# Kernel optimization log

Hardware: AMD Instinct MI355X
Metric: run time of the kernel (lower is better)

## Reference

```python
import jax, jax.numpy as jnp
import numpy as np

HID = 64


def _lstm_cell(x, h, c, Wih, Whh, bih, bhh):
    # gates: [B, 4*HID], PyTorch LSTMCell gate order: i, f, g, o
    gates = x @ Wih.T + bih + h @ Whh.T + bhh
    i, f, g, o = jnp.split(gates, 4, axis=-1)
    c_new = jax.nn.sigmoid(f) * c + jax.nn.sigmoid(i) * jnp.tanh(g)
    h_new = jax.nn.sigmoid(o) * jnp.tanh(c_new)
    return h_new, c_new


def setup_inputs() -> dict:
    key = jax.random.key(0)
    ks = jax.random.split(key, 11)
    B = 131072
    s_in2 = 1.0 / np.sqrt(2.0)
    s_h = 1.0 / np.sqrt(HID)
    return {
        "train_agent": jax.random.normal(ks[0], (B, 20, 2), jnp.float32),
        "enc_Wih": jax.random.uniform(ks[1], (4 * HID, 2), jnp.float32, -s_h, s_h),
        "enc_Whh": jax.random.uniform(ks[2], (4 * HID, HID), jnp.float32, -s_h, s_h),
        "enc_bih": jax.random.uniform(ks[3], (4 * HID,), jnp.float32, -s_h, s_h),
        "enc_bhh": jax.random.uniform(ks[4], (4 * HID,), jnp.float32, -s_h, s_h),
        "dec_Wih": jax.random.uniform(ks[5], (4 * HID, HID), jnp.float32, -s_h, s_h),
        "dec_Whh": jax.random.uniform(ks[6], (4 * HID, HID), jnp.float32, -s_h, s_h),
        "dec_bih": jax.random.uniform(ks[7], (4 * HID,), jnp.float32, -s_h, s_h),
        "dec_bhh": jax.random.uniform(ks[8], (4 * HID,), jnp.float32, -s_h, s_h),
        "lin_W": jax.random.uniform(ks[9], (2, HID), jnp.float32, -s_h, s_h),
        "lin_b": jax.random.uniform(ks[10], (2,), jnp.float32, -s_h, s_h),
    }


def reference(train_agent, enc_Wih, enc_Whh, enc_bih, enc_bhh,
              dec_Wih, dec_Whh, dec_bih, dec_bhh, lin_W, lin_b):
    B = train_agent.shape[0]
    h0 = jnp.zeros((B, HID), train_agent.dtype)
    c0 = jnp.zeros((B, HID), train_agent.dtype)

    # Encoder: 20 sequential LSTMCell steps over [B, 20, 2]
    def enc_step(carry, x_t):
        h, c = carry
        h, c = _lstm_cell(x_t, h, c, enc_Wih, enc_Whh, enc_bih, enc_bhh)
        return (h, c), None

    xs = jnp.swapaxes(train_agent, 0, 1)  # [20, B, 2]
    (h, c), _ = jax.lax.scan(enc_step, (h0, c0), xs)

    # Decoder: 30 steps, feeding h back in as input; emit Linear(h)
    def dec_step(carry, _):
        h, c = carry
        h, c = _lstm_cell(h, h, c, dec_Wih, dec_Whh, dec_bih, dec_bhh)
        out = h @ lin_W.T + lin_b  # [B, 2]
        return (h, c), out

    (_, _), outs = jax.lax.scan(dec_step, (h, c), None, length=30)
    return jnp.swapaxes(outs, 0, 1)  # [B, 30, 2]
```

## Files before the change

kernel.cpp:

```cpp
#include <hip/hip_runtime.h>


#define LOG2E 1.44269504088896340736f
#define TWO_LOG2E 2.88539008177792681472f

typedef __attribute__((ext_vector_type(4))) short short4v;
typedef __attribute__((ext_vector_type(4))) float float4v;
typedef __attribute__((ext_vector_type(4))) unsigned int uint4v;
typedef _Float16 __attribute__((ext_vector_type(8))) half8v;

#if defined(__HIP_DEVICE_COMPILE__)
#define MFMAH(a, b, c) __builtin_amdgcn_mfma_f32_16x16x32_f16((a), (b), (c), 0, 0, 0)
#else
#define MFMAH(a, b, c) (c)
#endif

__device__ __forceinline__ float4v exp2v4(float4v x) {
  float4v r;
  r[0] = __builtin_amdgcn_exp2f(x[0]);
  r[1] = __builtin_amdgcn_exp2f(x[1]);
  r[2] = __builtin_amdgcn_exp2f(x[2]);
  r[3] = __builtin_amdgcn_exp2f(x[3]);
  return r;
}
__device__ __forceinline__ float4v rcpv4(float4v x) {
  float4v r;
  r[0] = __builtin_amdgcn_rcpf(x[0]);
  r[1] = __builtin_amdgcn_rcpf(x[1]);
  r[2] = __builtin_amdgcn_rcpf(x[2]);
  r[3] = __builtin_amdgcn_rcpf(x[3]);
  return r;
}

__device__ __forceinline__ void cellact(const float4v* a, float4v& c,
                                        short4v& hh) {
  const float4v one = {1.f, 1.f, 1.f, 1.f};
  const float4v clo = {-36.f, -36.f, -36.f, -36.f};
  const float4v chi = {36.f, 36.f, 36.f, 36.f};
  float4v Ei = exp2v4(a[0]);
  float4v Ef = exp2v4(a[1]);
  float4v Eg = exp2v4(a[2]);
  float4v Eo = exp2v4(a[3]);
  float4v t1 = one + Ei;
  float4v t2 = one + Eg;
  float4v t3 = one + Ef;
  float4v t4s = Eg * TWO_LOG2E - TWO_LOG2E;
  float4v P = t1 * t2;
  float4v num = c * P + t4s * t3;
  float4v cs = num * rcpv4(P * t3);
  c = cs;
  float4v cl = __builtin_elementwise_min(__builtin_elementwise_max(cs, clo), chi);
  float4v Ec = exp2v4(cl);
  float4v h = (Ec - one) * rcpv4((one + Ec) * (one + Eo));
#pragma unroll
  for (int r = 0; r < 4; ++r) {
    _Float16 hf = (_Float16)h[r];
    hh[r] = (short)__builtin_bit_cast(unsigned short, hf);
  }
}

__global__ __launch_bounds__(256, 3) void lstm_fused(
    const float* __restrict__ x,
    const float* __restrict__ eWih,
    const float* __restrict__ eWhh,
    const float* __restrict__ ebih,
    const float* __restrict__ ebhh,
    const float* __restrict__ dWih,
    const float* __restrict__ dWhh,
    const float* __restrict__ dbih,
    const float* __restrict__ dbhh,
    const float* __restrict__ linW,
    const float* __restrict__ linb,
    float* __restrict__ out,
    int B) {
  const int tid = threadIdx.x;
  const int w   = tid >> 6;
  const int l   = tid & 63;
  const int m   = l & 15;
  const int tg  = l >> 4;
  const int msk = m & 14;
  const int wslot = (((w << 2) | tg) ^ msk) << 2;
  const int bg  = blockIdx.x * 32;

  __shared__ __align__(16) unsigned short WL[10][256][8];
  __shared__ __align__(16) unsigned short Hh[2][32][64];
  __shared__ unsigned int Xs16[32][21];

  const half8v hz8 = {0, 0, 0, 0, 0, 0, 0, 0};
  const float4v zf = {0.f, 0.f, 0.f, 0.f};

  {
    const size_t xoff = (size_t)blockIdx.x * 1280;
    for (int i = tid; i < 640; i += 256) {
      int mm = i / 20, st = i - mm * 20;
      size_t g = xoff + (size_t)mm * 40 + st * 2;
      float xa = 0.f, xb = 0.f;
      if (g + 1 < (size_t)B * 40) { xa = x[g]; xb = x[g + 1]; }
      unsigned ua = __builtin_bit_cast(unsigned short, (_Float16)xa);
      unsigned ub = __builtin_bit_cast(unsigned short, (_Float16)xb);
      Xs16[mm][st] = (ub << 16) | ua;
    }
  }

  half8v eA2[4];
#pragma unroll
  for (int gi = 0; gi < 4; ++gi) {
    const float gsc = (gi == 2) ? TWO_LOG2E : -LOG2E;
    const int nA = m + 16 * (4 * gi + w);
#pragma unroll
    for (int q = 0; q < 2; ++q) {
      const float* wp = &eWhh[nA * 64 + 32 * q + 8 * tg];
      float4v w0 = *(const float4v*)wp;
      float4v w1 = *(const float4v*)(wp + 4);
      half8v hi;
#pragma unroll
      for (int e = 0; e < 4; ++e) {
        hi[e]     = (_Float16)(w0[e] * gsc);
        hi[4 + e] = (_Float16)(w1[e] * gsc);
      }
      *(half8v*)&WL[gi * 2 + q][tid][0] = hi;
    }
    half8v a2 = hz8;
    if (tg == 0) {
      a2[0] = (_Float16)(eWih[nA * 2 + 0] * gsc);
      a2[1] = (_Float16)(eWih[nA * 2 + 1] * gsc);
      a2[2] = (_Float16)((ebih[nA] + ebhh[nA]) * gsc);
    }
    eA2[gi] = a2;
  }

  __syncthreads();

  float4v c0 = {0.f, 0.f, 0.f, 0.f}, c1 = {0.f, 0.f, 0.f, 0.f};
  half8v b0[2] = {hz8, hz8}, b1[2] = {hz8, hz8};
  int p = 0;

#pragma unroll 1
  for (int st = 0; st < 20; ++st) {
    short4v hh0, hh1;
    {
      uint4v t; t[0] = Xs16[m][st]; t[1] = 0x3C00u; t[2] = 0u; t[3] = 0u;
      half8v bq2 = (tg == 0) ? __builtin_bit_cast(half8v, t) : hz8;
      float4v a0[4];
#pragma unroll
      for (int gi = 0; gi < 4; ++gi) {
        half8v f0 = *(const half8v*)&WL[gi * 2 + 0][tid][0];
        half8v f1 = *(const half8v*)&WL[gi * 2 + 1][tid][0];
        float4v a = MFMAH(eA2[gi], bq2, zf);
        a = MFMAH(f0, b0[0], a);
        a0[gi] = MFMAH(f1, b0[1], a);
      }
      cellact(a0, c0, hh0);
    }
    {
      uint4v t; t[0] = Xs16[m + 16][st]; t[1] = 0x3C00u; t[2] = 0u; t[3] = 0u;
      half8v bq2 = (tg == 0) ? __builtin_bit_cast(half8v, t) : hz8;
      float4v a1[4];
#pragma unroll
      for (int gi = 0; gi < 4; ++gi) {
        half8v f0 = *(const half8v*)&WL[gi * 2 + 0][tid][0];
        half8v f1 = *(const half8v*)&WL[gi * 2 + 1][tid][0];
        float4v a = MFMAH(eA2[gi], bq2, zf);
        a = MFMAH(f0, b1[0], a);
        a1[gi] = MFMAH(f1, b1[1], a);
      }
      cellact(a1, c1, hh1);
    }
    *(short4v*)&Hh[p][m][wslot]      = hh0;
    *(short4v*)&Hh[p][m + 16][wslot] = hh1;
    __syncthreads();
#pragma unroll
    for (int q = 0; q < 2; ++q) {
      const int rs = (((8 * q) | (2 * tg)) ^ msk) << 2;
      b0[q] = *(const half8v*)&Hh[p][m][rs];
      b1[q] = *(const half8v*)&Hh[p][m + 16][rs];
    }
    p ^= 1;
  }

  float4v dbsv[4];
#pragma unroll
  for (int gi = 0; gi < 4; ++gi) {
    const float gsc = (gi == 2) ? TWO_LOG2E : -LOG2E;
    const int nA = m + 16 * (4 * gi + w);
#pragma unroll
    for (int q = 0; q < 2; ++q) {
      const float* wpa = &dWih[nA * 64 + 32 * q + 8 * tg];
      const float* wpb = &dWhh[nA * 64 + 32 * q + 8 * tg];
      float4v a0v = *(const float4v*)wpa;
      float4v a1v = *(const float4v*)(wpa + 4);
      float4v b0v = *(const float4v*)wpb;
      float4v b1v = *(const float4v*)(wpb + 4);
      half8v hi;
#pragma unroll
      for (int e = 0; e < 4; ++e) {
        hi[e]     = (_Float16)((a0v[e] + b0v[e]) * gsc);
        hi[4 + e] = (_Float16)((a1v[e] + b1v[e]) * gsc);
      }
      *(half8v*)&WL[gi * 2 + q][tid][0] = hi;
    }
#pragma unroll
    for (int r = 0; r < 4; ++r) {
      const int n = 64 * gi + 16 * w + 4 * tg + r;
      dbsv[gi][r] = (dbih[n] + dbhh[n]) * gsc;
    }
  }
#pragma unroll
  for (int q = 0; q < 2; ++q) {
    half8v hi = hz8;
    if (m < 2) {
      const int k0 = 32 * q + 8 * tg;
#pragma unroll
      for (int e = 0; e < 4; ++e) {
        hi[e]     = (_Float16)linW[m * 64 + k0 + e];
        hi[4 + e] = (_Float16)linW[m * 64 + k0 + e + 4];
      }
    }
    *(half8v*)&WL[8 + q][tid][0] = hi;
  }
  float4v lbinit = {0.f, 0.f, 0.f, 0.f};
  if (tg == 0) { lbinit[0] = linb[0]; lbinit[1] = linb[1]; }
  __syncthreads();

#pragma unroll 1
  for (int st = 0; st < 30; ++st) {
    short4v hh0, hh1;
    {
      float4v a0[4];
#pragma unroll
      for (int gi = 0; gi < 4; ++gi) {
        half8v f0 = *(const half8v*)&WL[gi * 2 + 0][tid][0];
        half8v f1 = *(const half8v*)&WL[gi * 2 + 1][tid][0];
        float4v a = MFMAH(f0, b0[0], dbsv[gi]);
        a0[gi] = MFMAH(f1, b0[1], a);
      }
      cellact(a0, c0, hh0);
    }
    {
      float4v a1[4];
#pragma unroll
      for (int gi = 0; gi < 4; ++gi) {
        half8v f0 = *(const half8v*)&WL[gi * 2 + 0][tid][0];
        half8v f1 = *(const half8v*)&WL[gi * 2 + 1][tid][0];
        float4v a = MFMAH(f0, b1[0], dbsv[gi]);
        a1[gi] = MFMAH(f1, b1[1], a);
      }
      cellact(a1, c1, hh1);
    }
    *(short4v*)&Hh[p][m][wslot]      = hh0;
    *(short4v*)&Hh[p][m + 16][wslot] = hh1;
    __syncthreads();
#pragma unroll
    for (int q = 0; q < 2; ++q) {
      const int rs = (((8 * q) | (2 * tg)) ^ msk) << 2;
      b0[q] = *(const half8v*)&Hh[p][m][rs];
      b1[q] = *(const half8v*)&Hh[p][m + 16][rs];
    }
    if (w == 0) {
      half8v L0 = *(const half8v*)&WL[8][tid][0];
      half8v L1 = *(const half8v*)&WL[9][tid][0];
      float4v la = lbinit;
      la = MFMAH(L0, b0[0], la);
      la = MFMAH(L1, b0[1], la);
      if (l < 16 && (bg + l) < B) {
        size_t oidx = ((size_t)(bg + l) * 30 + st) * 2;
        *(float2*)&out[oidx] = make_float2(la[0], la[1]);
      }
    } else if (w == 1) {
      half8v L0 = *(const half8v*)&WL[8][tid][0];
      half8v L1 = *(const half8v*)&WL[9][tid][0];
      float4v la = lbinit;
      la = MFMAH(L0, b1[0], la);
      la = MFMAH(L1, b1[1], la);
      if (l < 16 && (bg + 16 + l) < B) {
        size_t oidx = ((size_t)(bg + 16 + l) * 30 + st) * 2;
        *(float2*)&out[oidx] = make_float2(la[0], la[1]);
      }
    }
    p ^= 1;
  }
}

extern "C" void kernel_launch(void* const* d_in, const int* in_sizes, int n_in,
                              void* d_out, int out_size, void* d_ws, size_t ws_size,
                              hipStream_t stream) {
  (void)n_in; (void)out_size; (void)d_ws; (void)ws_size;
  const float* x    = (const float*)d_in[0];
  const float* eWih = (const float*)d_in[1];
  const float* eWhh = (const float*)d_in[2];
  const float* ebih = (const float*)d_in[3];
  const float* ebhh = (const float*)d_in[4];
  const float* dWih = (const float*)d_in[5];
  const float* dWhh = (const float*)d_in[6];
  const float* dbih = (const float*)d_in[7];
  const float* dbhh = (const float*)d_in[8];
  const float* linW = (const float*)d_in[9];
  const float* linb = (const float*)d_in[10];

  const int B = in_sizes[0] / 40;
  const int grid = (B + 31) / 32;
  lstm_fused<<<grid, 256, 0, stream>>>(x, eWih, eWhh, ebih, ebhh,
                                       dWih, dWhh, dbih, dbhh, linW, linb,
                                       (float*)d_out, B);
}
```

Measured before the change: 432.6 us.

## Halve per-block batch to 16 rows and raise occupancy to four blocks

Each 256-thread block now handles 16 batch rows instead of 32, so each wave runs one MFMA/cell chain per step instead of two. This lowers register pressure, and the launch bound is raised from 3 to 4 blocks per SM. Decoder biases move from registers to a shared-memory array, and the linear-layer weights move to a compact LDS table. The trade-off is twice as many blocks, each redoing the weight conversion into LDS, and less independent work per wave to hide MFMA and transcendental latency between barriers.

```diff
diff --git a/kernel.cpp b/kernel.cpp
--- a/kernel.cpp
+++ b/kernel.cpp
@@ -59,7 +59,7 @@
   }
 }
 
-__global__ __launch_bounds__(256, 3) void lstm_fused(
+__global__ __launch_bounds__(256, 4) void lstm_fused(
     const float* __restrict__ x,
     const float* __restrict__ eWih,
     const float* __restrict__ eWhh,
@@ -80,18 +80,20 @@
   const int tg  = l >> 4;
   const int msk = m & 14;
   const int wslot = (((w << 2) | tg) ^ msk) << 2;
-  const int bg  = blockIdx.x * 32;
-
-  __shared__ __align__(16) unsigned short WL[10][256][8];
-  __shared__ __align__(16) unsigned short Hh[2][32][64];
-  __shared__ unsigned int Xs16[32][21];
+  const int bg  = blockIdx.x * 16;
+
+  __shared__ __align__(16) unsigned short WL[8][256][8];
+  __shared__ __align__(16) unsigned short Hh[2][16][64];
+  __shared__ unsigned int Xs16[16][21];
+  __shared__ __align__(16) float dbsL[256];
+  __shared__ __align__(16) unsigned short LAc[2][64];
 
   const half8v hz8 = {0, 0, 0, 0, 0, 0, 0, 0};
   const float4v zf = {0.f, 0.f, 0.f, 0.f};
 
   {
-    const size_t xoff = (size_t)blockIdx.x * 1280;
-    for (int i = tid; i < 640; i += 256) {
+    const size_t xoff = (size_t)blockIdx.x * 640;
+    for (int i = tid; i < 320; i += 256) {
       int mm = i / 20, st = i - mm * 20;
       size_t g = xoff + (size_t)mm * 40 + st * 2;
       float xa = 0.f, xb = 0.f;
@@ -131,54 +133,35 @@
 
   __syncthreads();
 
-  float4v c0 = {0.f, 0.f, 0.f, 0.f}, c1 = {0.f, 0.f, 0.f, 0.f};
-  half8v b0[2] = {hz8, hz8}, b1[2] = {hz8, hz8};
+  float4v c0 = {0.f, 0.f, 0.f, 0.f};
+  half8v b0[2] = {hz8, hz8};
   int p = 0;
 
 #pragma unroll 1
   for (int st = 0; st < 20; ++st) {
-    short4v hh0, hh1;
-    {
-      uint4v t; t[0] = Xs16[m][st]; t[1] = 0x3C00u; t[2] = 0u; t[3] = 0u;
-      half8v bq2 = (tg == 0) ? __builtin_bit_cast(half8v, t) : hz8;
-      float4v a0[4];
-#pragma unroll
-      for (int gi = 0; gi < 4; ++gi) {
-        half8v f0 = *(const half8v*)&WL[gi * 2 + 0][tid][0];
-        half8v f1 = *(const half8v*)&WL[gi * 2 + 1][tid][0];
-        float4v a = MFMAH(eA2[gi], bq2, zf);
-        a = MFMAH(f0, b0[0], a);
-        a0[gi] = MFMAH(f1, b0[1], a);
-      }
-      cellact(a0, c0, hh0);
-    }
-    {
-      uint4v t; t[0] = Xs16[m + 16][st]; t[1] = 0x3C00u; t[2] = 0u; t[3] = 0u;
-      half8v bq2 = (tg == 0) ? __builtin_bit_cast(half8v, t) : hz8;
-      float4v a1[4];
-#pragma unroll
-      for (int gi = 0; gi < 4; ++gi) {
-        half8v f0 = *(const half8v*)&WL[gi * 2 + 0][tid][0];
-        half8v f1 = *(const half8v*)&WL[gi * 2 + 1][tid][0];
-        float4v a = MFMAH(eA2[gi], bq2, zf);
-        a = MFMAH(f0, b1[0], a);
-        a1[gi] = MFMAH(f1, b1[1], a);
-      }
-      cellact(a1, c1, hh1);
-    }
-    *(short4v*)&Hh[p][m][wslot]      = hh0;
-    *(short4v*)&Hh[p][m + 16][wslot] = hh1;
+    uint4v t; t[0] = Xs16[m][st]; t[1] = 0x3C00u; t[2] = 0u; t[3] = 0u;
+    half8v bq2 = __builtin_bit_cast(half8v, t);
+    float4v a0[4];
+#pragma unroll
+    for (int gi = 0; gi < 4; ++gi) {
+      half8v f0 = *(const half8v*)&WL[gi * 2 + 0][tid][0];
+      half8v f1 = *(const half8v*)&WL[gi * 2 + 1][tid][0];
+      float4v a = MFMAH(eA2[gi], bq2, zf);
+      a = MFMAH(f0, b0[0], a);
+      a0[gi] = MFMAH(f1, b0[1], a);
+    }
+    short4v hh0;
+    cellact(a0, c0, hh0);
+    *(short4v*)&Hh[p][m][wslot] = hh0;
     __syncthreads();
 #pragma unroll
     for (int q = 0; q < 2; ++q) {
       const int rs = (((8 * q) | (2 * tg)) ^ msk) << 2;
       b0[q] = *(const half8v*)&Hh[p][m][rs];
-      b1[q] = *(const half8v*)&Hh[p][m + 16][rs];
     }
     p ^= 1;
   }
 
-  float4v dbsv[4];
 #pragma unroll
   for (int gi = 0; gi < 4; ++gi) {
     const float gsc = (gi == 2) ? TWO_LOG2E : -LOG2E;
@@ -199,24 +182,11 @@
       }
       *(half8v*)&WL[gi * 2 + q][tid][0] = hi;
     }
-#pragma unroll
-    for (int r = 0; r < 4; ++r) {
-      const int n = 64 * gi + 16 * w + 4 * tg + r;
-      dbsv[gi][r] = (dbih[n] + dbhh[n]) * gsc;
-    }
-  }
-#pragma unroll
-  for (int q = 0; q < 2; ++q) {
-    half8v hi = hz8;
-    if (m < 2) {
-      const int k0 = 32 * q + 8 * tg;
-#pragma unroll
-      for (int e = 0; e < 4; ++e) {
-        hi[e]     = (_Float16)linW[m * 64 + k0 + e];
-        hi[4 + e] = (_Float16)linW[m * 64 + k0 + e + 4];
-      }
-    }
-    *(half8v*)&WL[8 + q][tid][0] = hi;
+  }
+  dbsL[tid] = (dbih[tid] + dbhh[tid]) * (((tid >> 6) == 2) ? TWO_LOG2E : -LOG2E);
+  if (tid < 128) {
+    LAc[tid >> 6][tid & 63] =
+        __builtin_bit_cast(unsigned short, (_Float16)linW[tid]);
   }
   float4v lbinit = {0.f, 0.f, 0.f, 0.f};
   if (tg == 0) { lbinit[0] = linb[0]; lbinit[1] = linb[1]; }
@@ -224,56 +194,33 @@
 
 #pragma unroll 1
   for (int st = 0; st < 30; ++st) {
-    short4v hh0, hh1;
-    {
-      float4v a0[4];
-#pragma unroll
-      for (int gi = 0; gi < 4; ++gi) {
-        half8v f0 = *(const half8v*)&WL[gi * 2 + 0][tid][0];
-        half8v f1 = *(const half8v*)&WL[gi * 2 + 1][tid][0];
-        float4v a = MFMAH(f0, b0[0], dbsv[gi]);
-        a0[gi] = MFMAH(f1, b0[1], a);
-      }
-      cellact(a0, c0, hh0);
-    }
-    {
-      float4v a1[4];
-#pragma unroll
-      for (int gi = 0; gi < 4; ++gi) {
-        half8v f0 = *(const half8v*)&WL[gi * 2 + 0][tid][0];
-        half8v f1 = *(const half8v*)&WL[gi * 2 + 1][tid][0];
-        float4v a = MFMAH(f0, b1[0], dbsv[gi]);
-        a1[gi] = MFMAH(f1, b1[1], a);
-      }
-      cellact(a1, c1, hh1);
-    }
-    *(short4v*)&Hh[p][m][wslot]      = hh0;
-    *(short4v*)&Hh[p][m + 16][wslot] = hh1;
+    float4v a0[4];
+#pragma unroll
+    for (int gi = 0; gi < 4; ++gi) {
+      half8v f0 = *(const half8v*)&WL[gi * 2 + 0][tid][0];
+      half8v f1 = *(const half8v*)&WL[gi * 2 + 1][tid][0];
+      float4v ci = *(const float4v*)&dbsL[64 * gi + 16 * w + 4 * tg];
+      float4v a = MFMAH(f0, b0[0], ci);
+      a0[gi] = MFMAH(f1, b0[1], a);
+    }
+    short4v hh0;
+    cellact(a0, c0, hh0);
+    *(short4v*)&Hh[p][m][wslot] = hh0;
     __syncthreads();
 #pragma unroll
     for (int q = 0; q < 2; ++q) {
       const int rs = (((8 * q) | (2 * tg)) ^ msk) << 2;
       b0[q] = *(const half8v*)&Hh[p][m][rs];
-      b1[q] = *(const half8v*)&Hh[p][m + 16][rs];
     }
     if (w == 0) {
-      half8v L0 = *(const half8v*)&WL[8][tid][0];
-      half8v L1 = *(const half8v*)&WL[9][tid][0];
       float4v la = lbinit;
-      la = MFMAH(L0, b0[0], la);
-      la = MFMAH(L1, b0[1], la);
+#pragma unroll
+      for (int q = 0; q < 2; ++q) {
+        half8v LAq = *(const half8v*)&LAc[m & 1][32 * q + 8 * tg];
+        la = MFMAH(LAq, b0[q], la);
+      }
       if (l < 16 && (bg + l) < B) {
         size_t oidx = ((size_t)(bg + l) * 30 + st) * 2;
-        *(float2*)&out[oidx] = make_float2(la[0], la[1]);
-      }
-    } else if (w == 1) {
-      half8v L0 = *(const half8v*)&WL[8][tid][0];
-      half8v L1 = *(const half8v*)&WL[9][tid][0];
-      float4v la = lbinit;
-      la = MFMAH(L0, b1[0], la);
-      la = MFMAH(L1, b1[1], la);
-      if (l < 16 && (bg + 16 + l) < B) {
-        size_t oidx = ((size_t)(bg + 16 + l) * 30 + st) * 2;
         *(float2*)&out[oidx] = make_float2(la[0], la[1]);
       }
     }
@@ -298,7 +245,7 @@
   const float* linb = (const float*)d_in[10];
 
   const int B = in_sizes[0] / 40;
-  const int grid = (B + 31) / 32;
+  const int grid = (B + 15) / 16;
   lstm_fused<<<grid, 256, 0, stream>>>(x, eWih, eWhh, ebih, ebhh,
                                        dWih, dWhh, dbih, dbhh, linW, linb,
                                        (float*)d_out, B);
```

Result: slower. 475.9 us (+10.0%).
